# Performance work log

Hardware: AMD Instinct MI355X
Metric: run time of the kernel (lower is better)

Reference implementation:

```python
import jax, jax.numpy as jnp
import numpy as np
from jax import lax

# dims: batch, depth, height, width, in-channels
B, D, H, W, C = 1, 48, 48, 48, 8
K = 3          # cubic kernel size
R = 2          # n_radial_profiles = K//2 + 1
DEG = 3        # max_degree
NH = (DEG + 1) ** 2   # n_harmonics = 16
OUT = 16       # out_channels (filters)


def setup_inputs() -> dict:
    key = jax.random.key(0)
    ks = jax.random.split(key, 6)
    return {
        "x": jax.random.normal(ks[0], (B, D, H, W, C), jnp.float32),
        "atoms_real": jax.random.normal(ks[1], (K, K, K, R, NH), jnp.float32),
        "atoms_imag": jax.random.normal(ks[2], (K, K, K, R, NH), jnp.float32),
        "w": jax.random.normal(ks[3], (C, OUT, R, DEG + 1), jnp.float32) * 0.1,
        "w_center": jax.random.normal(ks[4], (C, OUT), jnp.float32) * 0.1,
        "b_center": jnp.zeros((OUT,), jnp.float32),
    }


def _depthwise_sh_conv(x, filt):
    # x: [B,D,H,W,C]; filt: [K,K,K,R,NH].  The torch code loops conv3d per input
    # channel with the SAME [K,K,K,1,R*NH] filter bank; that is exactly a
    # depthwise conv with channel multiplier R*NH and a tiled kernel.
    k = filt.shape[0]
    r, nh = filt.shape[3], filt.shape[4]
    c = x.shape[-1]
    kern = jnp.tile(filt.reshape(k, k, k, 1, r * nh), (1, 1, 1, 1, c))  # [K,K,K,1,C*R*NH], c-major
    dn = lax.conv_dimension_numbers(x.shape, kern.shape, ("NDHWC", "DHWIO", "NDHWC"))
    y = lax.conv_general_dilated(x, kern, (1, 1, 1), "SAME",
                                 dimension_numbers=dn, feature_group_count=c)
    # -> [B,D,H,W,C,R,NH]
    return y.reshape(x.shape[:4] + (c, r, nh))


def reference(x, atoms_real, atoms_imag, w, w_center, b_center):
    deg = w.shape[-1] - 1
    # repeat_interleave of per-degree weights over the 2k+1 orders of each degree
    idx = np.repeat(np.arange(deg + 1), [2 * n + 1 for n in range(deg + 1)])  # [NH]
    w_exp = w[..., idx]  # [C, OUT, R, NH]

    feat_r = _depthwise_sh_conv(x, atoms_real)  # [B,D,H,W,C,R,NH]
    feat_i = _depthwise_sh_conv(x, atoms_imag)

    # weighted reduction over input channels (axis 4) and radial profiles (axis 6)
    real = jnp.einsum("bdhwcrn,cfrn->bdhwfn", feat_r, w_exp)
    imag = jnp.einsum("bdhwcrn,cfrn->bdhwfn", feat_i, w_exp)

    # central-pixel 1x1x1 conv added to harmonic index 0 of the real part
    central = jnp.einsum("bdhwc,cf->bdhwf", x, w_center) + b_center
    real = real.at[..., 0].add(central)

    # stack real/imag feature maps: [B,D,H,W,OUT,NH,2]
    return jnp.stack([real, imag], axis=-1)
```

## Files before the change

### kernel.cpp

```cpp
#include <hip/hip_runtime.h>


typedef _Float16 half8_t __attribute__((ext_vector_type(8)));
typedef float floatx4 __attribute__((ext_vector_type(4)));

#define TB_SLOTS (7 * 32 * 64)
#define TBL_BYTES (TB_SLOTS * 16)
#define XP_OFF   TBL_BYTES
#define XP_BYTES (50 * 50 * 50 * 16)
#define BIAS_OFF (XP_OFF + XP_BYTES)
#define WS_T4_BYTES (BIAS_OFF + 16)
#define WS_T3_BYTES TBL_BYTES

typedef __attribute__((address_space(1))) const unsigned int gq_t;
typedef __attribute__((address_space(3))) unsigned int lq_t;

__device__ inline unsigned short f2h(float v) {
    return __builtin_bit_cast(unsigned short, (_Float16)v);
}
__device__ inline unsigned pk2(float a, float b) {
    return (unsigned)f2h(a) | ((unsigned)f2h(b) << 16);
}

__global__ __launch_bounds__(512) void bsh_precompute_gemm(
    const float* __restrict__ AR,
    const float* __restrict__ AI,
    const float* __restrict__ Wgt,
    const float* __restrict__ WC,
    const float* __restrict__ Bc,
    uint4* __restrict__ TB)
{
    int s = blockIdx.x * 512 + threadIdx.x;
    if (s >= TB_SLOTS) return;
    int l = s & 63, ot = (s >> 6) & 31, t = s >> 11;
    int col = 16 * ot + (l & 15);
    int f = col >> 5, n = (col >> 1) & 15, ri = col & 1;
    int dg = (n >= 9) ? 3 : (n >= 4) ? 2 : (n >= 1) ? 1 : 0;
    const float* atom = ri ? AI : AR;
    float vj[8];
    #pragma unroll
    for (int j = 0; j < 8; ++j) {
        int kap = 32 * t + 8 * (l >> 4) + j;
        int k = kap >> 3, c = kap & 7;
        float v = 0.f;
        if (k < 27) {
            float w0 = Wgt[((c * 16 + f) * 2 + 0) * 4 + dg];
            float w1 = Wgt[((c * 16 + f) * 2 + 1) * 4 + dg];
            v = atom[k * 32 + n] * w0 + atom[k * 32 + 16 + n] * w1;
            if (k == 13 && n == 0 && ri == 0) v += WC[c * 16 + f];
        } else {
            if (c == 7 && n == 0 && ri == 0) v = Bc[f];
        }
        vj[j] = v;
    }
    TB[s] = make_uint4(pk2(vj[0], vj[1]), pk2(vj[2], vj[3]),
                       pk2(vj[4], vj[5]), pk2(vj[6], vj[7]));
}

__global__ __launch_bounds__(512) void bsh_xp(
    const float* __restrict__ X, char* __restrict__ WSB)
{
    int idx = blockIdx.x * 512 + threadIdx.x;
    if (idx == 0)
        *(uint4*)(WSB + BIAS_OFF) = make_uint4(0u, 0u, 0u, 0x3C000000u);
    if (idx >= 125000) return;
    int dd = idx / 2500, rem = idx - dd * 2500;
    int hh = rem / 50, ww = rem - hh * 50;
    unsigned x01 = 0, x23 = 0, x45 = 0, x67 = 0;
    if (dd >= 1 && dd <= 48 && hh >= 1 && hh <= 48 && ww >= 1 && ww <= 48) {
        const float* px = &X[((((dd - 1) * 48) + (hh - 1)) * 48 + (ww - 1)) * 8];
        float4 a = *(const float4*)px;
        float4 b = *(const float4*)(px + 4);
        x01 = pk2(a.x, a.y); x23 = pk2(a.z, a.w);
        x45 = pk2(b.x, b.y); x67 = pk2(b.z, b.w);
    }
    *(uint4*)(WSB + XP_OFF + (size_t)idx * 16) = make_uint4(x01, x23, x45, x67);
}

__global__ __launch_bounds__(512) void bsh_gemm_t4(
    const char* __restrict__ WSB,
    float* __restrict__ Out)
{
    __shared__ __align__(16) _Float16 B_lds[2][28 * 48 * 8];

    const int tid = threadIdx.x;
    const int bid = blockIdx.x;
    const int nb = bid & 1;
    const int rb = bid >> 1;
    const int d  = rb / 24;
    const int hp = rb - 24 * d;

    const uint4* TB   = (const uint4*)WSB;
    const char*  Xp   = WSB + XP_OFF;
    const char*  BIAS = WSB + BIAS_OFF;

    const int lane = tid & 63, cg = tid >> 6;
    const int kg = lane >> 4, lr = lane & 15;

    const uint4* ap = TB + ((size_t)(nb * 16 + cg * 2) * 64 + lane);
    uint4 af[2][7];
    #pragma unroll
    for (int t = 0; t < 7; ++t) {
        af[0][t] = ap[(size_t)(t * 32 + 0) * 64];
        af[1][t] = ap[(size_t)(t * 32 + 1) * 64];
    }

    auto stage = [&](int hf) {
        #pragma unroll
        for (int i = 0; i < 3; ++i) {
            int cell = tid + i * 512;
            if (cell < 1344) {
                int k = cell / 48;
                int v = cell - 48 * k;
                const char* src;
                if (k == 27) {
                    src = BIAS;
                } else {
                    int kz = k / 9, r9 = k - 9 * kz;
                    int ky = r9 / 3, kx = r9 - 3 * ky;
                    int dd  = d + kz;
                    int hhp = 2 * hp + hf + ky;
                    int wwp = v + kx;
                    src = Xp + (((size_t)(dd * 50 + hhp) * 50 + wwp) << 4);
                }
                __builtin_amdgcn_global_load_lds(
                    (const gq_t*)src,
                    (lq_t*)&B_lds[hf][cell * 8],
                    16, 0, 0);
            }
        }
    };

    auto compute = [&](int hf) {
        const char* bbase = (const char*)&B_lds[hf][0] + kg * 768 + lr * 16;
        #pragma unroll 1
        for (int vt = 0; vt < 3; ++vt) {
            const char* brow = bbase + vt * 256;
            half8_t b[7];
            #pragma unroll
            for (int t = 0; t < 7; ++t)
                b[t] = *(const half8_t*)(brow + t * 3072);

            floatx4 a0 = (floatx4){0.f, 0.f, 0.f, 0.f};
            floatx4 a1 = (floatx4){0.f, 0.f, 0.f, 0.f};
            #pragma unroll
            for (int t = 0; t < 7; ++t)
                a0 = __builtin_amdgcn_mfma_f32_16x16x32_f16(
                         __builtin_bit_cast(half8_t, af[0][t]), b[t], a0, 0, 0, 0);
            #pragma unroll
            for (int t = 0; t < 7; ++t)
                a1 = __builtin_amdgcn_mfma_f32_16x16x32_f16(
                         __builtin_bit_cast(half8_t, af[1][t]), b[t], a1, 0, 0, 0);

            float* ob = Out + (size_t)((d * 48 + 2 * hp + hf) * 48 + vt * 16 + lr) * 512
                            + nb * 256 + cg * 32 + 4 * kg;
            *(floatx4*)ob        = a0;
            *(floatx4*)(ob + 16) = a1;
        }
    };

    stage(0);
    __syncthreads();
    stage(1);
    compute(0);
    __syncthreads();
    compute(1);
}

__global__ __launch_bounds__(512) void bsh_gemm_t3(
    const float* __restrict__ X,
    const uint4* __restrict__ TB,
    float* __restrict__ Out)
{
    __shared__ _Float16 B_lds[96 * 232];

    const int tid = threadIdx.x;
    const int bid = blockIdx.x;
    const int nb = bid & 1;
    const int rb = bid >> 1;
    const int d  = rb / 24;
    const int hp = rb - 24 * d;

    const int lane = tid & 63, cg = tid >> 6;
    const int kg = lane >> 4, lr = lane & 15;

    const uint4* ap = TB + ((size_t)(nb * 16 + cg * 2) * 64 + lane);
    uint4 af[2][7];
    #pragma unroll
    for (int t = 0; t < 7; ++t) {
        af[0][t] = ap[(size_t)(t * 32 + 0) * 64];
        af[1][t] = ap[(size_t)(t * 32 + 1) * 64];
    }

    #pragma unroll
    for (int i = 0; i < 6; ++i) {
        int cell = tid + i * 512;
        if (cell < 2688) {
            int k = cell / 96;
            int v = cell - 96 * k;
            unsigned x01 = 0, x23 = 0, x45 = 0, x67 = 0;
            if (k == 27) {
                x67 = 0x3C000000u;
            } else {
                int kz = k / 9, r9 = k - 9 * kz;
                int ky = r9 / 3, kx = r9 - 3 * ky;
                int hl = (v >= 48) ? 1 : 0;
                int dd = d - 1 + kz;
                int hh = 2 * hp + hl - 1 + ky;
                int ww = v - 48 * hl - 1 + kx;
                if ((unsigned)dd < 48u && (unsigned)hh < 48u && (unsigned)ww < 48u) {
                    const float* px = &X[(((dd * 48 + hh) * 48) + ww) * 8];
                    float4 a = *(const float4*)px;
                    float4 b = *(const float4*)(px + 4);
                    x01 = pk2(a.x, a.y); x23 = pk2(a.z, a.w);
                    x45 = pk2(b.x, b.y); x67 = pk2(b.z, b.w);
                }
            }
            char* wp = (char*)B_lds + v * 464 + k * 16;
            *(uint2*)wp       = make_uint2(x01, x23);
            *(uint2*)(wp + 8) = make_uint2(x45, x67);
        }
    }
    __syncthreads();

    const char* bbase = (const char*)B_lds + lr * 464 + kg * 16;

    #pragma unroll 1
    for (int vt = 0; vt < 6; ++vt) {
        const char* brow = bbase + (size_t)vt * 16 * 464;
        half8_t b[7];
        #pragma unroll
        for (int t = 0; t < 7; ++t)
            b[t] = *(const half8_t*)(brow + 64 * t);

        floatx4 a0 = (floatx4){0.f, 0.f, 0.f, 0.f};
        floatx4 a1 = (floatx4){0.f, 0.f, 0.f, 0.f};
        #pragma unroll
        for (int t = 0; t < 7; ++t)
            a0 = __builtin_amdgcn_mfma_f32_16x16x32_f16(
                     __builtin_bit_cast(half8_t, af[0][t]), b[t], a0, 0, 0, 0);
        #pragma unroll
        for (int t = 0; t < 7; ++t)
            a1 = __builtin_amdgcn_mfma_f32_16x16x32_f16(
                     __builtin_bit_cast(half8_t, af[1][t]), b[t], a1, 0, 0, 0);

        float* ob = Out + (size_t)(rb * 96 + vt * 16 + lr) * 512
                        + nb * 256 + cg * 32 + 4 * kg;
        *(floatx4*)ob        = a0;
        *(floatx4*)(ob + 16) = a1;
    }
}

#define FB_NBLK (48*48*6)
#define FB_WS_FLOATS 5968

__global__ __launch_bounds__(512) void fb_precompute(
    const float* __restrict__ AR, const float* __restrict__ AI,
    const float* __restrict__ Wgt, const float* __restrict__ WC,
    const float* __restrict__ Bc, float* __restrict__ T)
{
    const int tid = threadIdx.x;
    for (int i = tid; i < 4096; i += 512) {
        int row = i >> 4, f = row >> 4, n = row & 15;
        int pc = (i >> 2) & 3, e = i & 3;
        int chunk = pc ^ (n & 3);
        int cr = chunk * 4 + e, c = cr >> 1, r = cr & 1;
        int dg = (n >= 9) ? 3 : (n >= 4) ? 2 : (n >= 1) ? 1 : 0;
        T[i] = Wgt[c * 128 + f * 8 + r * 4 + dg];
    }
    for (int i = tid; i < 1728; i += 512) {
        int k = i >> 6, n = (i >> 2) & 15, q = i & 3;
        const float* src = (q >> 1) ? AI : AR;
        T[4096 + i] = src[k * 32 + (q & 1) * 16 + n];
    }
    if (tid < 128) T[5824 + tid] = WC[(tid & 7) * 16 + (tid >> 3)];
    if (tid < 16)  T[5952 + tid] = Bc[tid];
}

__device__ inline float4 fb_shfl_xor4(float4 v, int m) {
    return make_float4(__shfl_xor(v.x, m), __shfl_xor(v.y, m),
                       __shfl_xor(v.z, m), __shfl_xor(v.w, m));
}

__global__ __launch_bounds__(512) void fb_kernel(
    const float* __restrict__ X, const float* __restrict__ T,
    float* __restrict__ Out)
{
    __shared__ float cst[FB_WS_FLOATS];
    __shared__ float x_lds[720];

    const int tid = threadIdx.x;
    const int bid = blockIdx.x;
    const int d  = bid / (48 * 6);
    const int r0 = bid - d * (48 * 6);
    const int h  = r0 / 6;
    const int w0 = (r0 - h * 6) * 8;

    {
        const float4* t4 = (const float4*)T;
        float4* c4 = (float4*)cst;
        #pragma unroll
        for (int i = 0; i < 3; ++i) {
            int idx = tid + i * 512;
            if (idx < FB_WS_FLOATS / 4) c4[idx] = t4[idx];
        }
        if (tid < 180) {
            int r3 = tid / 20, rem = tid - r3 * 20;
            int wx = rem >> 1, c0 = (rem & 1) * 4;
            int dz = r3 / 3, dy = r3 - dz * 3;
            int dd = d - 1 + dz, hh = h - 1 + dy, ww = w0 - 1 + wx;
            float4 v = make_float4(0.f, 0.f, 0.f, 0.f);
            if ((unsigned)dd < 48u && (unsigned)hh < 48u && (unsigned)ww < 48u)
                v = *(const float4*)&X[(((dd * 48 + hh) * 48 + ww) * 8) + c0];
            *(float4*)&x_lds[tid * 4] = v;
        }
    }
    __syncthreads();

    const int wave = tid >> 6, lane = tid & 63;
    const int n = lane & 15, g = lane >> 4;
    const float* atoms_lds = cst + 4096;
    const float* wc_lds    = cst + 5824;
    const float* b_lds     = cst + 5952;

    float sr0 = 0, sr1 = 0, sr2 = 0, sr3 = 0;
    float si0 = 0, si1 = 0, si2 = 0, si3 = 0;
    #pragma unroll
    for (int kz = 0; kz < 3; ++kz)
    #pragma unroll
    for (int ky = 0; ky < 3; ++ky)
    #pragma unroll
    for (int kx = 0; kx < 3; ++kx) {
        const int k = (kz * 3 + ky) * 3 + kx;
        const float2 xv = *(const float2*)&x_lds[(((kz * 3 + ky) * 10) + wave + kx) * 8 + 2 * g];
        const float4 a  = *(const float4*)&atoms_lds[k * 64 + n * 4];
        sr0 += xv.x * a.x; sr1 += xv.x * a.y;
        sr2 += xv.y * a.x; sr3 += xv.y * a.y;
        si0 += xv.x * a.z; si1 += xv.x * a.w;
        si2 += xv.y * a.z; si3 += xv.y * a.w;
    }
    const float4 sR0 = make_float4(sr0, sr1, sr2, sr3);
    const float4 sI0 = make_float4(si0, si1, si2, si3);
    const float4 sR1 = fb_shfl_xor4(sR0, 16), sI1 = fb_shfl_xor4(sI0, 16);
    const float4 sR2 = fb_shfl_xor4(sR0, 32), sI2 = fb_shfl_xor4(sI0, 32);
    const float4 sR3 = fb_shfl_xor4(sR1, 32), sI3 = fb_shfl_xor4(sI1, 32);

    float cent[4];
    {
        const int cb = ((1 * 3 + 1) * 10 + wave + 1) * 8;
        const float4 xc0 = *(const float4*)&x_lds[cb];
        const float4 xc1 = *(const float4*)&x_lds[cb + 4];
        #pragma unroll
        for (int fi = 0; fi < 4; ++fi) {
            const int f = 4 * g + fi;
            const float* wcr = &wc_lds[f * 8];
            cent[fi] = b_lds[f]
                + xc0.x * wcr[0] + xc0.y * wcr[1] + xc0.z * wcr[2] + xc0.w * wcr[3]
                + xc1.x * wcr[4] + xc1.y * wcr[5] + xc1.z * wcr[6] + xc1.w * wcr[7];
        }
    }

    const float4* w4 = (const float4*)cst;
    const int gx = g ^ (n & 3);
    const int out_base = ((d * 48 + h) * 48 + (w0 + wave)) * 512;
    #pragma unroll
    for (int fi = 0; fi < 4; ++fi) {
        const int f = 4 * g + fi;
        const int rb2 = (f * 16 + n) * 4;
        const float4 w0v = w4[rb2 + (gx ^ 0)];
        const float4 w1v = w4[rb2 + (gx ^ 1)];
        const float4 w2v = w4[rb2 + (gx ^ 2)];
        const float4 w3v = w4[rb2 + (gx ^ 3)];
        float accR = w0v.x*sR0.x + w0v.y*sR0.y + w0v.z*sR0.z + w0v.w*sR0.w
                   + w1v.x*sR1.x + w1v.y*sR1.y + w1v.z*sR1.z + w1v.w*sR1.w
                   + w2v.x*sR2.x + w2v.y*sR2.y + w2v.z*sR2.z + w2v.w*sR2.w
                   + w3v.x*sR3.x + w3v.y*sR3.y + w3v.z*sR3.z + w3v.w*sR3.w;
        float accI = w0v.x*sI0.x + w0v.y*sI0.y + w0v.z*sI0.z + w0v.w*sI0.w
                   + w1v.x*sI1.x + w1v.y*sI1.y + w1v.z*sI1.z + w1v.w*sI1.w
                   + w2v.x*sI2.x + w2v.y*sI2.y + w2v.z*sI2.z + w2v.w*sI2.w
                   + w3v.x*sI3.x + w3v.y*sI3.y + w3v.z*sI3.z + w3v.w*sI3.w;
        if (n == 0) accR += cent[fi];
        *(float2*)&Out[out_base + (f * 16 + n) * 2] = make_float2(accR, accI);
    }
}

extern "C" void kernel_launch(void* const* d_in, const int* in_sizes, int n_in,
                              void* d_out, int out_size, void* d_ws, size_t ws_size,
                              hipStream_t stream) {
    (void)in_sizes; (void)n_in; (void)out_size;
    const float* x  = (const float*)d_in[0];
    const float* ar = (const float*)d_in[1];
    const float* ai = (const float*)d_in[2];
    const float* w  = (const float*)d_in[3];
    const float* wc = (const float*)d_in[4];
    const float* bc = (const float*)d_in[5];
    float* out = (float*)d_out;

    if (ws_size >= (size_t)WS_T4_BYTES) {
        char* wsb = (char*)d_ws;
        hipLaunchKernelGGL(bsh_precompute_gemm, dim3(28), dim3(512), 0, stream,
                           ar, ai, w, wc, bc, (uint4*)wsb);
        hipLaunchKernelGGL(bsh_xp, dim3(245), dim3(512), 0, stream, x, wsb);
        hipLaunchKernelGGL(bsh_gemm_t4, dim3(2304), dim3(512), 0, stream,
                           (const char*)wsb, out);
    } else if (ws_size >= (size_t)WS_T3_BYTES) {
        uint4* tb = (uint4*)d_ws;
        hipLaunchKernelGGL(bsh_precompute_gemm, dim3(28), dim3(512), 0, stream,
                           ar, ai, w, wc, bc, tb);
        hipLaunchKernelGGL(bsh_gemm_t3, dim3(2304), dim3(512), 0, stream,
                           x, tb, out);
    } else {
        float* tbl = (float*)d_ws;
        hipLaunchKernelGGL(fb_precompute, dim3(1), dim3(512), 0, stream,
                           ar, ai, w, wc, bc, tbl);
        hipLaunchKernelGGL(fb_kernel, dim3(FB_NBLK), dim3(512), 0, stream,
                           x, tbl, out);
    }
}
```

Before: 54.65 us.

## Process three row-pairs per block with cross-tile double-buffered staging

The main GEMM kernel now has each block loop over three consecutive row-pair tiles instead of one, cutting the grid from 2304 to 768 blocks. The A-fragment register loads are amortized over three tiles, and staging of the next tile's first half is overlapped with computing the current tile's second half. This trades fewer blocks (less parallelism and latency hiding across CUs) for less per-block setup and weight reloading.

Result: faster. 51.77 us (-5.3%).

```diff
diff --git a/kernel.cpp b/kernel.cpp
--- a/kernel.cpp
+++ b/kernel.cpp
@@ -9,7 +9,7 @@
 #define XP_OFF   TBL_BYTES
 #define XP_BYTES (50 * 50 * 50 * 16)
 #define BIAS_OFF (XP_OFF + XP_BYTES)
-#define WS_T4_BYTES (BIAS_OFF + 16)
+#define WS_T5_BYTES (BIAS_OFF + 16)
 #define WS_T3_BYTES TBL_BYTES
 
 typedef __attribute__((address_space(1))) const unsigned int gq_t;
@@ -77,7 +77,7 @@
     *(uint4*)(WSB + XP_OFF + (size_t)idx * 16) = make_uint4(x01, x23, x45, x67);
 }
 
-__global__ __launch_bounds__(512) void bsh_gemm_t4(
+__global__ __launch_bounds__(512) void bsh_gemm_t5(
     const char* __restrict__ WSB,
     float* __restrict__ Out)
 {
@@ -86,9 +86,7 @@
     const int tid = threadIdx.x;
     const int bid = blockIdx.x;
     const int nb = bid & 1;
-    const int rb = bid >> 1;
-    const int d  = rb / 24;
-    const int hp = rb - 24 * d;
+    const int g3 = (bid >> 1) * 3;
 
     const uint4* TB   = (const uint4*)WSB;
     const char*  Xp   = WSB + XP_OFF;
@@ -105,7 +103,9 @@
         af[1][t] = ap[(size_t)(t * 32 + 1) * 64];
     }
 
-    auto stage = [&](int hf) {
+    auto stage = [&](int hf, int rb) {
+        int d  = rb / 24;
+        int hp = rb - 24 * d;
         #pragma unroll
         for (int i = 0; i < 3; ++i) {
             int cell = tid + i * 512;
@@ -131,7 +131,9 @@
         }
     };
 
-    auto compute = [&](int hf) {
+    auto compute = [&](int hf, int rb) {
+        int d  = rb / 24;
+        int hp = rb - 24 * d;
         const char* bbase = (const char*)&B_lds[hf][0] + kg * 768 + lr * 16;
         #pragma unroll 1
         for (int vt = 0; vt < 3; ++vt) {
@@ -159,12 +161,18 @@
         }
     };
 
-    stage(0);
+    stage(0, g3);
     __syncthreads();
-    stage(1);
-    compute(0);
-    __syncthreads();
-    compute(1);
+    #pragma unroll 1
+    for (int ti = 0; ti < 3; ++ti) {
+        int rb = g3 + ti;
+        stage(1, rb);
+        compute(0, rb);
+        __syncthreads();
+        if (ti < 2) stage(0, rb + 1);
+        compute(1, rb);
+        __syncthreads();
+    }
 }
 
 __global__ __launch_bounds__(512) void bsh_gemm_t3(
@@ -396,12 +404,12 @@
     const float* bc = (const float*)d_in[5];
     float* out = (float*)d_out;
 
-    if (ws_size >= (size_t)WS_T4_BYTES) {
+    if (ws_size >= (size_t)WS_T5_BYTES) {
         char* wsb = (char*)d_ws;
         hipLaunchKernelGGL(bsh_precompute_gemm, dim3(28), dim3(512), 0, stream,
                            ar, ai, w, wc, bc, (uint4*)wsb);
         hipLaunchKernelGGL(bsh_xp, dim3(245), dim3(512), 0, stream, x, wsb);
-        hipLaunchKernelGGL(bsh_gemm_t4, dim3(2304), dim3(512), 0, stream,
+        hipLaunchKernelGGL(bsh_gemm_t5, dim3(768), dim3(512), 0, stream,
                            (const char*)wsb, out);
     } else if (ws_size >= (size_t)WS_T3_BYTES) {
         uint4* tb = (uint4*)d_ws;
```

## Load im2col B fragments directly from global and process six rows per block

Applied to the files above, without the earlier changes.

The GEMM kernel no longer stages im2col tiles into LDS through global_load_lds with barriers. Each lane now computes its kernel-tap offsets once and reads its B fragments straight from the padded fp16 input buffer in global memory. Each block covers six output rows instead of two, so the grid shrinks from 2304 to 768 blocks and the A fragments held in registers are reused over more rows. The cost is global, cache-served loads in place of shared-memory reads, and fewer blocks available to hide memory latency.

Measured after the change: 69.33 us. 26.8% more time.

```diff
diff --git a/kernel.cpp b/kernel.cpp
--- a/kernel.cpp
+++ b/kernel.cpp
@@ -9,7 +9,7 @@
 #define XP_OFF   TBL_BYTES
 #define XP_BYTES (50 * 50 * 50 * 16)
 #define BIAS_OFF (XP_OFF + XP_BYTES)
-#define WS_T4_BYTES (BIAS_OFF + 16)
+#define WS_T6_BYTES (BIAS_OFF + 16)
 #define WS_T3_BYTES TBL_BYTES
 
 typedef __attribute__((address_space(1))) const unsigned int gq_t;
@@ -77,94 +77,76 @@
     *(uint4*)(WSB + XP_OFF + (size_t)idx * 16) = make_uint4(x01, x23, x45, x67);
 }
 
-__global__ __launch_bounds__(512) void bsh_gemm_t4(
+__global__ __launch_bounds__(512) void bsh_gemm_t6(
     const char* __restrict__ WSB,
     float* __restrict__ Out)
 {
-    __shared__ __align__(16) _Float16 B_lds[2][28 * 48 * 8];
-
     const int tid = threadIdx.x;
     const int bid = blockIdx.x;
     const int nb = bid & 1;
-    const int rb = bid >> 1;
-    const int d  = rb / 24;
-    const int hp = rb - 24 * d;
-
-    const uint4* TB   = (const uint4*)WSB;
-    const char*  Xp   = WSB + XP_OFF;
-    const char*  BIAS = WSB + BIAS_OFF;
+    const int m  = bid >> 1;
+    const int g3 = m * 3;
+    const int d  = g3 / 24;
+    const int hbase = 2 * (g3 - 24 * d);
+
+    const uint4* TB = (const uint4*)WSB;
+    const char*  Xp = WSB + XP_OFF;
 
     const int lane = tid & 63, cg = tid >> 6;
     const int kg = lane >> 4, lr = lane & 15;
 
     const uint4* ap = TB + ((size_t)(nb * 16 + cg * 2) * 64 + lane);
-    uint4 af[2][7];
+    uint4 af0[7], af1[7];
     #pragma unroll
     for (int t = 0; t < 7; ++t) {
-        af[0][t] = ap[(size_t)(t * 32 + 0) * 64];
-        af[1][t] = ap[(size_t)(t * 32 + 1) * 64];
-    }
-
-    auto stage = [&](int hf) {
-        #pragma unroll
-        for (int i = 0; i < 3; ++i) {
-            int cell = tid + i * 512;
-            if (cell < 1344) {
-                int k = cell / 48;
-                int v = cell - 48 * k;
-                const char* src;
-                if (k == 27) {
-                    src = BIAS;
-                } else {
-                    int kz = k / 9, r9 = k - 9 * kz;
-                    int ky = r9 / 3, kx = r9 - 3 * ky;
-                    int dd  = d + kz;
-                    int hhp = 2 * hp + hf + ky;
-                    int wwp = v + kx;
-                    src = Xp + (((size_t)(dd * 50 + hhp) * 50 + wwp) << 4);
-                }
-                __builtin_amdgcn_global_load_lds(
-                    (const gq_t*)src,
-                    (lq_t*)&B_lds[hf][cell * 8],
-                    16, 0, 0);
+        af0[t] = ap[(size_t)(t * 32 + 0) * 64];
+        af1[t] = ap[(size_t)(t * 32 + 1) * 64];
+    }
+
+    int ko[7];
+    #pragma unroll
+    for (int t = 0; t < 7; ++t) {
+        int k = 4 * t + kg;
+        if (k > 27) k = 27;
+        int kz = k / 9, r9 = k - 9 * kz;
+        int ky = r9 / 3, kx = r9 - 3 * ky;
+        ko[t] = (kz * 2500 + ky * 50 + kx) * 16;
+    }
+    const bool isbias = (kg == 3);
+
+    #pragma unroll 1
+    for (int hs = 0; hs < 6; ++hs) {
+        const int h = hbase + hs;
+        const int rowvoff = (d * 2500 + h * 50 + lr) * 16;
+        #pragma unroll 1
+        for (int ws2 = 0; ws2 < 3; ++ws2) {
+            const int sb = rowvoff + ws2 * 256;
+            uint4 b[7];
+            #pragma unroll
+            for (int t = 0; t < 7; ++t) {
+                int off = sb + ko[t];
+                if (t == 6 && isbias) off = XP_BYTES;
+                b[t] = *(const uint4*)(Xp + off);
             }
-        }
-    };
-
-    auto compute = [&](int hf) {
-        const char* bbase = (const char*)&B_lds[hf][0] + kg * 768 + lr * 16;
-        #pragma unroll 1
-        for (int vt = 0; vt < 3; ++vt) {
-            const char* brow = bbase + vt * 256;
-            half8_t b[7];
-            #pragma unroll
-            for (int t = 0; t < 7; ++t)
-                b[t] = *(const half8_t*)(brow + t * 3072);
-
             floatx4 a0 = (floatx4){0.f, 0.f, 0.f, 0.f};
             floatx4 a1 = (floatx4){0.f, 0.f, 0.f, 0.f};
             #pragma unroll
             for (int t = 0; t < 7; ++t)
                 a0 = __builtin_amdgcn_mfma_f32_16x16x32_f16(
-                         __builtin_bit_cast(half8_t, af[0][t]), b[t], a0, 0, 0, 0);
+                         __builtin_bit_cast(half8_t, af0[t]),
+                         __builtin_bit_cast(half8_t, b[t]), a0, 0, 0, 0);
             #pragma unroll
             for (int t = 0; t < 7; ++t)
                 a1 = __builtin_amdgcn_mfma_f32_16x16x32_f16(
-                         __builtin_bit_cast(half8_t, af[1][t]), b[t], a1, 0, 0, 0);
-
-            float* ob = Out + (size_t)((d * 48 + 2 * hp + hf) * 48 + vt * 16 + lr) * 512
+                         __builtin_bit_cast(half8_t, af1[t]),
+                         __builtin_bit_cast(half8_t, b[t]), a1, 0, 0, 0);
+
+            float* ob = Out + (size_t)((d * 48 + h) * 48 + ws2 * 16 + lr) * 512
                             + nb * 256 + cg * 32 + 4 * kg;
             *(floatx4*)ob        = a0;
             *(floatx4*)(ob + 16) = a1;
         }
-    };
-
-    stage(0);
-    __syncthreads();
-    stage(1);
-    compute(0);
-    __syncthreads();
-    compute(1);
+    }
 }
 
 __global__ __launch_bounds__(512) void bsh_gemm_t3(
@@ -396,12 +378,12 @@
     const float* bc = (const float*)d_in[5];
     float* out = (float*)d_out;
 
-    if (ws_size >= (size_t)WS_T4_BYTES) {
+    if (ws_size >= (size_t)WS_T6_BYTES) {
         char* wsb = (char*)d_ws;
         hipLaunchKernelGGL(bsh_precompute_gemm, dim3(28), dim3(512), 0, stream,
                            ar, ai, w, wc, bc, (uint4*)wsb);
         hipLaunchKernelGGL(bsh_xp, dim3(245), dim3(512), 0, stream, x, wsb);
-        hipLaunchKernelGGL(bsh_gemm_t4, dim3(2304), dim3(512), 0, stream,
+        hipLaunchKernelGGL(bsh_gemm_t6, dim3(768), dim3(512), 0, stream,
                            (const char*)wsb, out);
     } else if (ws_size >= (size_t)WS_T3_BYTES) {
         uint4* tb = (uint4*)d_ws;
```
